# Kernel tuning notes

Measured on AMD Instinct MI355X. Metric: run time of the kernel, lower is better.

## Reference

```python
import jax, jax.numpy as jnp
import numpy as np

NUM_GRAPHS = 512
BN_EPS = 1e-5

def _lin(k, fin, fout):
    kw, kb = jax.random.split(k)
    s = 1.0 / np.sqrt(fin)
    return (jax.random.uniform(kw, (fin, fout), jnp.float32, -s, s),
            jax.random.uniform(kb, (fout,), jnp.float32, -s, s))

def setup_inputs() -> dict:
    key = jax.random.key(0)
    ks = jax.random.split(key, 16)
    N, E, F, C, H, O = 50000, 800000, 128, 256, 512, 768
    x = jax.random.normal(ks[0], (N, F), jnp.float32)
    edge_index = jax.random.randint(ks[1], (2, E), 0, N, jnp.int64)
    batch = jnp.sort(jax.random.randint(ks[2], (N,), 0, NUM_GRAPHS, jnp.int64))
    d = {"x": x, "edge_index": edge_index, "batch": batch}
    d["w1a"], d["b1a"] = _lin(ks[3], F, C)
    d["g1"], d["be1"] = jnp.ones((C,), jnp.float32), jnp.zeros((C,), jnp.float32)
    d["w1b"], d["b1b"] = _lin(ks[4], C, C)
    d["w2a"], d["b2a"] = _lin(ks[5], C, C)
    d["g2"], d["be2"] = jnp.ones((C,), jnp.float32), jnp.zeros((C,), jnp.float32)
    d["w2b"], d["b2b"] = _lin(ks[6], C, C)
    d["w3a"], d["b3a"] = _lin(ks[7], C, C)
    d["g3"], d["be3"] = jnp.ones((C,), jnp.float32), jnp.zeros((C,), jnp.float32)
    d["w3b"], d["b3b"] = _lin(ks[8], C, C)
    d["wh1"], d["bh1"] = _lin(ks[9], C, H)
    d["wh2"], d["bh2"] = _lin(ks[10], H, O)
    return d

def _bn(z, g, b):
    mu = jnp.mean(z, axis=0)
    var = jnp.mean((z - mu) ** 2, axis=0)  # biased var, torch BN training mode
    return (z - mu) * jax.lax.rsqrt(var + BN_EPS) * g + b

def _gin(x, edge_index, wa, ba, g, be, wb, bb, tanh_out):
    src, dst = edge_index[0], edge_index[1]
    agg = jax.ops.segment_sum(x[src], dst, num_segments=x.shape[0])
    h = x + agg  # eps = 0
    z = jax.nn.relu(_bn(h @ wa + ba, g, be))
    z = z @ wb + bb
    return jnp.tanh(z) if tanh_out else z

def reference(x, edge_index, batch,
              w1a, b1a, g1, be1, w1b, b1b,
              w2a, b2a, g2, be2, w2b, b2b,
              w3a, b3a, g3, be3, w3b, b3b,
              wh1, bh1, wh2, bh2):
    h = jax.nn.relu(_gin(x, edge_index, w1a, b1a, g1, be1, w1b, b1b, False))
    h = jax.nn.relu(_gin(h, edge_index, w2a, b2a, g2, be2, w2b, b2b, True))
    h = _gin(h, edge_index, w3a, b3a, g3, be3, w3b, b3b, True)
    # global mean pool over graphs
    sums = jax.ops.segment_sum(h, batch, num_segments=NUM_GRAPHS)
    cnt = jax.ops.segment_sum(jnp.ones((h.shape[0],), h.dtype), batch, num_segments=NUM_GRAPHS)
    pooled = sums / jnp.maximum(cnt, 1.0)[:, None]
    z = jax.nn.relu(pooled @ wh1 + bh1)
    return z @ wh2 + bh2
```

## Files before the change

kernel.cpp:

```cpp
#include <hip/hip_runtime.h>


typedef __attribute__((ext_vector_type(8))) short short8;
typedef __attribute__((ext_vector_type(4))) float f32x4;
typedef __attribute__((ext_vector_type(4))) unsigned short us4;
typedef __attribute__((ext_vector_type(8))) unsigned short us8;

__device__ __forceinline__ unsigned short f2bf(float f) {
  unsigned int b = __float_as_uint(f);
  unsigned int r = 0x7FFFu + ((b >> 16) & 1u);
  return (unsigned short)((b + r) >> 16);
}
__device__ __forceinline__ float bf2f(unsigned short u) {
  return __uint_as_float(((unsigned int)u) << 16);
}

__device__ __forceinline__ int sw8(int row) {
  return (row & 7) ^ ((row >> 3) & 7);
}

typedef const __attribute__((address_space(1))) unsigned int* gas1;
typedef __attribute__((address_space(3))) unsigned int* las3;
__device__ __forceinline__ void gload16(const void* g, void* l) {
  __builtin_amdgcn_global_load_lds((gas1)g, (las3)l, 16, 0, 0);
}

__device__ __forceinline__ size_t swz8_idx(int row, int k, int K) {
  int g = k >> 3;
  return (size_t)row * K + ((g >> 3) << 6) + ((((g & 7) ^ sw8(row)) << 3)) + (k & 7);
}

__global__ void k_histbounds(const int* __restrict__ ei, int* __restrict__ deg, int E,
                             int eb, const int* __restrict__ batch,
                             int* __restrict__ gs, int* __restrict__ ge, int N) {
  int b = blockIdx.x;
  if (b < eb) {
    int e = b * 256 + threadIdx.x;
    if (e < E) atomicAdd(&deg[ei[E + e]], 1);
  } else {
    int i = (b - eb) * 256 + threadIdx.x;
    if (i < N) {
      int bb = batch[i];
      if (i == 0 || batch[i - 1] != bb) gs[bb] = i;
      if (i == N - 1 || batch[i + 1] != bb) ge[bb] = i + 1;
    }
  }
}

__global__ __launch_bounds__(1024) void k_scan1(const int* __restrict__ deg,
                                                int* __restrict__ partial,
                                                int* __restrict__ bsum, int N) {
  __shared__ int sd[1024];
  int tid = threadIdx.x;
  int i = blockIdx.x * 1024 + tid;
  int v = (i < N) ? deg[i] : 0;
  sd[tid] = v;
  __syncthreads();
  for (int off = 1; off < 1024; off <<= 1) {
    int t = (tid >= off) ? sd[tid - off] : 0;
    __syncthreads();
    sd[tid] += t;
    __syncthreads();
  }
  if (i < N) partial[i] = sd[tid];
  if (tid == 1023) bsum[blockIdx.x] = sd[1023];
}

__global__ void k_scan2(int* __restrict__ bsum, int nb) {
  int l = threadIdx.x;
  int orig = (l < nb) ? bsum[l] : 0;
  int v = orig;
  for (int off = 1; off < 64; off <<= 1) {
    int t = __shfl_up(v, off);
    if (l >= off) v += t;
  }
  if (l < nb) bsum[l] = v - orig;
}

__global__ void k_scan3(const int* __restrict__ deg, const int* __restrict__ partial,
                        const int* __restrict__ bsum, int* __restrict__ rowptr,
                        int* __restrict__ cursor, int N) {
  int i = blockIdx.x * 256 + threadIdx.x;
  if (i >= N) return;
  int incl = partial[i] + bsum[i >> 10];
  rowptr[i + 1] = incl;
  cursor[i] = incl - deg[i];
  if (i == 0) rowptr[0] = 0;
}

__global__ void k_fill(const int* __restrict__ ei, int* __restrict__ cursor,
                       int* __restrict__ adj, int E) {
  int e = blockIdx.x * 256 + threadIdx.x;
  if (e >= E) return;
  int s = ei[e];
  int d = ei[E + e];
  int pos = atomicAdd(&cursor[d], 1);
  adj[pos] = s;
}

__global__ void k_xbf(const float* __restrict__ X, unsigned short* __restrict__ Xb,
                      int total) {
  int t = blockIdx.x * 256 + threadIdx.x;
  if (t * 8 >= total) return;
  const float4 v0 = *(const float4*)(X + t * 8);
  const float4 v1 = *(const float4*)(X + t * 8 + 4);
  us8 o;
  o[0] = f2bf(v0.x); o[1] = f2bf(v0.y); o[2] = f2bf(v0.z); o[3] = f2bf(v0.w);
  o[4] = f2bf(v1.x); o[5] = f2bf(v1.y); o[6] = f2bf(v1.z); o[7] = f2bf(v1.w);
  *(us8*)(Xb + t * 8) = o;
}

__global__ void k_prep_all(const float* __restrict__ w1a, const float* __restrict__ w1b,
                           const float* __restrict__ w2a, const float* __restrict__ w2b,
                           const float* __restrict__ w3a, const float* __restrict__ w3b,
                           const float* __restrict__ wh1, const float* __restrict__ wh2,
                           unsigned short* __restrict__ Hi, unsigned short* __restrict__ Lo) {
  int idx = blockIdx.x * 256 + threadIdx.x;
  const float* W; int K, Nout, lo_;
  if (idx < 32768)       { W = w1a; K = 128; Nout = 256; lo_ = 0; }
  else if (idx < 98304)  { W = w1b; K = 256; Nout = 256; lo_ = 32768; }
  else if (idx < 163840) { W = w2a; K = 256; Nout = 256; lo_ = 98304; }
  else if (idx < 229376) { W = w2b; K = 256; Nout = 256; lo_ = 163840; }
  else if (idx < 294912) { W = w3a; K = 256; Nout = 256; lo_ = 229376; }
  else if (idx < 360448) { W = w3b; K = 256; Nout = 256; lo_ = 294912; }
  else if (idx < 491520) { W = wh1; K = 256; Nout = 512; lo_ = 360448; }
  else                   { W = wh2; K = 512; Nout = 768; lo_ = 491520; }
  int li = idx - lo_;
  int n = li % Nout, k = li / Nout;
  float w = W[k * Nout + n];
  unsigned short h = f2bf(w);
  size_t oi = (size_t)lo_ + swz8_idx(n, k, K);
  Hi[oi] = h;
  Lo[oi] = f2bf(w - bf2f(h));
}

template <int C>
__global__ __launch_bounds__(256) void k_agg(const unsigned short* __restrict__ Xb,
                                             unsigned short* __restrict__ Hb,
                                             const int* __restrict__ rowptr,
                                             const int* __restrict__ adj, int N,
                                             float* __restrict__ statsZ) {
  if (blockIdx.x == 0) {
    statsZ[threadIdx.x] = 0.f;
    statsZ[256 + threadIdx.x] = 0.f;
  }
  int node = blockIdx.x * 4 + (threadIdx.x >> 6);
  if (node >= N) return;
  int lane = threadIdx.x & 63;
  int e0 = rowptr[node], e1 = rowptr[node + 1];
  if constexpr (C == 256) {
    us4 ov = *(const us4*)(Xb + (size_t)node * C + lane * 4);
    float a0 = bf2f(ov[0]), a1 = bf2f(ov[1]), a2 = bf2f(ov[2]), a3 = bf2f(ov[3]);
    int e = e0;
    for (; e + 4 <= e1; e += 4) {
      int s0 = adj[e], s1 = adj[e + 1], s2 = adj[e + 2], s3 = adj[e + 3];
      us4 v0 = *(const us4*)(Xb + (size_t)s0 * C + lane * 4);
      us4 v1 = *(const us4*)(Xb + (size_t)s1 * C + lane * 4);
      us4 v2 = *(const us4*)(Xb + (size_t)s2 * C + lane * 4);
      us4 v3 = *(const us4*)(Xb + (size_t)s3 * C + lane * 4);
      a0 += (bf2f(v0[0]) + bf2f(v1[0])) + (bf2f(v2[0]) + bf2f(v3[0]));
      a1 += (bf2f(v0[1]) + bf2f(v1[1])) + (bf2f(v2[1]) + bf2f(v3[1]));
      a2 += (bf2f(v0[2]) + bf2f(v1[2])) + (bf2f(v2[2]) + bf2f(v3[2]));
      a3 += (bf2f(v0[3]) + bf2f(v1[3])) + (bf2f(v2[3]) + bf2f(v3[3]));
    }
    for (; e < e1; ++e) {
      us4 v = *(const us4*)(Xb + (size_t)adj[e] * C + lane * 4);
      a0 += bf2f(v[0]); a1 += bf2f(v[1]); a2 += bf2f(v[2]); a3 += bf2f(v[3]);
    }
    us4 hv;
    hv[0] = f2bf(a0); hv[1] = f2bf(a1); hv[2] = f2bf(a2); hv[3] = f2bf(a3);
    size_t oi = (size_t)node * 256 + ((lane >> 4) << 6) +
                ((((lane >> 1) & 7) ^ sw8(node)) << 3) + ((lane & 1) << 2);
    *(us4*)(Hb + oi) = hv;
  } else {
    ushort2 ov = *(const ushort2*)(Xb + (size_t)node * C + lane * 2);
    float a0 = bf2f(ov.x), a1 = bf2f(ov.y);
    int e = e0;
    for (; e + 4 <= e1; e += 4) {
      int s0 = adj[e], s1 = adj[e + 1], s2 = adj[e + 2], s3 = adj[e + 3];
      ushort2 v0 = *(const ushort2*)(Xb + (size_t)s0 * C + lane * 2);
      ushort2 v1 = *(const ushort2*)(Xb + (size_t)s1 * C + lane * 2);
      ushort2 v2 = *(const ushort2*)(Xb + (size_t)s2 * C + lane * 2);
      ushort2 v3 = *(const ushort2*)(Xb + (size_t)s3 * C + lane * 2);
      a0 += (bf2f(v0.x) + bf2f(v1.x)) + (bf2f(v2.x) + bf2f(v3.x));
      a1 += (bf2f(v0.y) + bf2f(v1.y)) + (bf2f(v2.y) + bf2f(v3.y));
    }
    for (; e < e1; ++e) {
      ushort2 v = *(const ushort2*)(Xb + (size_t)adj[e] * C + lane * 2);
      a0 += bf2f(v.x); a1 += bf2f(v.y);
    }
    ushort2 hv = {f2bf(a0), f2bf(a1)};
    size_t oi = (size_t)node * 128 + ((lane >> 5) << 6) +
                ((((lane >> 2) & 7) ^ sw8(node)) << 3) + ((lane & 3) << 1);
    *(ushort2*)(Hb + oi) = hv;
  }
}

template <int EPI, bool STATS, bool OSPLIT, bool XSWZ, int ASRC, bool FULL, bool OBF16>
__global__ __launch_bounds__(256) void k_gemm(
    const unsigned short* __restrict__ AHb, const unsigned short* __restrict__ ALo,
    const unsigned short* __restrict__ Zb,
    int M, int K, int Nld, int mb, int per,
    const unsigned short* __restrict__ WHi, const unsigned short* __restrict__ WLo,
    const float* __restrict__ bias,
    const float* __restrict__ statsIn, const float* __restrict__ gvec,
    const float* __restrict__ bevec,
    float* __restrict__ Out, unsigned short* __restrict__ OutB,
    unsigned short* __restrict__ OHi, unsigned short* __restrict__ OLo,
    float* __restrict__ statsOut) {
  __shared__ unsigned short aHi[4096], bHi[8192];
  __shared__ unsigned short aLo[FULL ? 4096 : 64], bLo[FULL ? 8192 : 64];
  __shared__ float sBNsc[ASRC == 2 ? 256 : 1], sBNsh[ASRC == 2 ? 256 : 1];
  int bx, by;
  if constexpr (XSWZ) {
    int xcd = blockIdx.x & 7, slot = blockIdx.x >> 3;
    bx = xcd * per + (slot >> 1);
    by = slot & 1;
    if (bx >= mb) return;
  } else {
    bx = blockIdx.x;
    by = blockIdx.y;
  }
  const int tid = threadIdx.x;
  const int lane = tid & 63, w = tid >> 6;
  const int wm = w >> 1, wn = w & 1;
  const int m0 = bx * 64, n0 = by * 128;

  if constexpr (ASRC == 2) {
    float mu = statsIn[tid] / (float)M;
    float var = statsIn[256 + tid] / (float)M - mu * mu;
    float sc = gvec[tid] * rsqrtf(var + 1e-5f);
    sBNsc[tid] = sc;
    sBNsh[tid] = bevec[tid] - mu * sc;
  }

  f32x4 zero = {0.f, 0.f, 0.f, 0.f};
  f32x4 acc[2][4];
#pragma unroll
  for (int i = 0; i < 2; ++i)
#pragma unroll
    for (int j = 0; j < 4; ++j) acc[i][j] = zero;

  const int l8 = lane >> 3;
  const int s8 = lane & 7;

  us8 zr0, zr1;
  const unsigned short* zb0 = nullptr;
  const unsigned short* zb1 = nullptr;
  if constexpr (ASRC == 2) {
    int r0 = tid >> 3, r1 = 32 + (tid >> 3);
    int ra0 = m0 + r0; if (ra0 >= M) ra0 = M - 1;
    int ra1 = m0 + r1; if (ra1 >= M) ra1 = M - 1;
    zb0 = Zb + (size_t)ra0 * K + (tid & 7) * 8;
    zb1 = Zb + (size_t)ra1 * K + (tid & 7) * 8;
    zr0 = *(const us8*)(zb0);
    zr1 = *(const us8*)(zb1);
  }

  for (int kb = 0; kb < K; kb += 64) {
    __syncthreads();
    if constexpr (ASRC == 2) {
#pragma unroll
      for (int p = 0; p < 2; ++p) {
        int row = (p << 5) + (tid >> 3), gq = tid & 7;
        us8 zr = p ? zr1 : zr0;
        us8 hv;
#pragma unroll
        for (int jj = 0; jj < 8; ++jj) {
          int kc = kb + gq * 8 + jj;
          float o = fmaxf(bf2f(zr[jj]) * sBNsc[kc] + sBNsh[kc], 0.f);
          hv[jj] = f2bf(o);
        }
        int bo = row * 128 + ((gq ^ sw8(row)) << 4);
        *(us8*)((char*)aHi + bo) = hv;
      }
#pragma unroll
      for (int q = 0; q < 4; ++q) {
        int row = (w << 5) + (q << 3) + l8;
        size_t gb = (size_t)(n0 + row) * K + kb + s8 * 8;
        unsigned bo2 = (w << 12) + (q << 10);
        gload16(WHi + gb, (char*)bHi + bo2);
      }
    } else {
#pragma unroll
      for (int q = 0; q < 2; ++q) {
        int row = (w << 4) + (q << 3) + l8;
        int ra = m0 + row; if (ra >= M) ra = M - 1;
        size_t ga = (size_t)ra * K + kb + s8 * 8;
        unsigned boA = (w << 11) + (q << 10);
        gload16(AHb + ga, (char*)aHi + boA);
        if constexpr (FULL) gload16(ALo + ga, (char*)aLo + boA);
      }
#pragma unroll
      for (int q = 0; q < 4; ++q) {
        int row = (w << 5) + (q << 3) + l8;
        size_t gb = (size_t)(n0 + row) * K + kb + s8 * 8;
        unsigned bo2 = (w << 12) + (q << 10);
        gload16(WHi + gb, (char*)bHi + bo2);
        if constexpr (FULL) gload16(WLo + gb, (char*)bLo + bo2);
      }
    }
    __syncthreads();

    if constexpr (ASRC == 2) {
      if (kb + 64 < K) {
        zr0 = *(const us8*)(zb0 + kb + 64);
        zr1 = *(const us8*)(zb1 + kb + 64);
      }
    }

    const int j = lane >> 4;
#pragma unroll
    for (int kk = 0; kk < 2; ++kk) {
      int g = (kk << 2) + j;
      short8 bh[4], bl[4];
#pragma unroll
      for (int ni = 0; ni < 4; ++ni) {
        int r = wn * 64 + ni * 16 + (lane & 15);
        int bo = r * 128 + ((g ^ sw8(r)) << 4);
        bh[ni] = *(const short8*)((const char*)bHi + bo);
        if constexpr (FULL) bl[ni] = *(const short8*)((const char*)bLo + bo);
      }
#pragma unroll
      for (int mi = 0; mi < 2; ++mi) {
        int r = wm * 32 + mi * 16 + (lane & 15);
        int bo = r * 128 + ((g ^ sw8(r)) << 4);
        short8 ah = *(const short8*)((const char*)aHi + bo);
#pragma unroll
        for (int ni = 0; ni < 4; ++ni) {
          acc[mi][ni] = __builtin_amdgcn_mfma_f32_16x16x32_bf16(ah, bh[ni], acc[mi][ni], 0, 0, 0);
          if constexpr (FULL) {
            short8 al = *(const short8*)((const char*)aLo + bo);
            acc[mi][ni] = __builtin_amdgcn_mfma_f32_16x16x32_bf16(ah, bl[ni], acc[mi][ni], 0, 0, 0);
            acc[mi][ni] = __builtin_amdgcn_mfma_f32_16x16x32_bf16(al, bh[ni], acc[mi][ni], 0, 0, 0);
          }
        }
      }
    }
  }

#pragma unroll
  for (int ni = 0; ni < 4; ++ni) {
    int col = n0 + wn * 64 + ni * 16 + (lane & 15);
    float bc = bias[col];
    float s = 0.f, q = 0.f;
#pragma unroll
    for (int mi = 0; mi < 2; ++mi) {
      int rbase = m0 + wm * 32 + mi * 16 + (lane >> 4) * 4;
#pragma unroll
      for (int r = 0; r < 4; ++r) {
        int row = rbase + r;
        if (row < M) {
          float o = acc[mi][ni][r] + bc;
          if (STATS) { s += o; q += o * o; }
          if (OSPLIT) {
            o = fmaxf(o, 0.f);
            unsigned short h = f2bf(o);
            size_t oi = swz8_idx(row, col, Nld);
            OHi[oi] = h;
            OLo[oi] = f2bf(o - bf2f(h));
          } else {
            if (EPI == 1) o = fmaxf(o, 0.f);
            else if (EPI == 2) o = tanhf(o);
            else if (EPI == 3) o = fmaxf(tanhf(o), 0.f);
            if (OBF16) OutB[(size_t)row * Nld + col] = f2bf(o);
            else       Out[(size_t)row * Nld + col] = o;
          }
        }
      }
    }
    if (STATS) {
      s += __shfl_xor(s, 16); s += __shfl_xor(s, 32);
      q += __shfl_xor(q, 16); q += __shfl_xor(q, 32);
      if ((lane >> 4) == 0) {
        atomicAdd(&statsOut[col], s);
        atomicAdd(&statsOut[256 + col], q);
      }
    }
  }
}

__global__ __launch_bounds__(256) void k_pool(const unsigned short* __restrict__ Hb,
                                              const int* __restrict__ gs,
                                              const int* __restrict__ ge,
                                              unsigned short* __restrict__ PHi,
                                              unsigned short* __restrict__ PLo) {
  __shared__ float4 red[4][64];
  int gi = blockIdx.x;
  int s = gs[gi], e = ge[gi];
  int w = threadIdx.x >> 6, lane = threadIdx.x & 63;
  float4 acc = {0.f, 0.f, 0.f, 0.f};
  for (int r = s + w; r < e; r += 4) {
    us4 v = *(const us4*)(Hb + (size_t)r * 256 + lane * 4);
    acc.x += bf2f(v[0]); acc.y += bf2f(v[1]);
    acc.z += bf2f(v[2]); acc.w += bf2f(v[3]);
  }
  red[w][lane] = acc;
  __syncthreads();
  if (w == 0) {
    float4 a = red[0][lane], b = red[1][lane], c = red[2][lane], d = red[3][lane];
    float inv = 1.0f / fmaxf((float)(e - s), 1.0f);
    float vv[4] = {(a.x + b.x + c.x + d.x) * inv, (a.y + b.y + c.y + d.y) * inv,
                   (a.z + b.z + c.z + d.z) * inv, (a.w + b.w + c.w + d.w) * inv};
    us4 hv, lv;
#pragma unroll
    for (int j = 0; j < 4; ++j) {
      unsigned short h = f2bf(vv[j]);
      hv[j] = h;
      lv[j] = f2bf(vv[j] - bf2f(h));
    }
    size_t oi = (size_t)gi * 256 + ((lane >> 4) << 6) +
                ((((lane >> 1) & 7) ^ sw8(gi)) << 3) + ((lane & 1) << 2);
    *(us4*)(PHi + oi) = hv;
    *(us4*)(PLo + oi) = lv;
  }
}

extern "C" void kernel_launch(void* const* d_in, const int* in_sizes, int n_in,
                              void* d_out, int out_size, void* d_ws, size_t ws_size,
                              hipStream_t stream) {
  const float* x      = (const float*)d_in[0];
  const int* ei       = (const int*)d_in[1];
  const int* bat      = (const int*)d_in[2];
  const float* w1a = (const float*)d_in[3];  const float* b1a = (const float*)d_in[4];
  const float* g1  = (const float*)d_in[5];  const float* be1 = (const float*)d_in[6];
  const float* w1b = (const float*)d_in[7];  const float* b1b = (const float*)d_in[8];
  const float* w2a = (const float*)d_in[9];  const float* b2a = (const float*)d_in[10];
  const float* g2  = (const float*)d_in[11]; const float* be2 = (const float*)d_in[12];
  const float* w2b = (const float*)d_in[13]; const float* b2b = (const float*)d_in[14];
  const float* w3a = (const float*)d_in[15]; const float* b3a = (const float*)d_in[16];
  const float* g3  = (const float*)d_in[17]; const float* be3 = (const float*)d_in[18];
  const float* w3b = (const float*)d_in[19]; const float* b3b = (const float*)d_in[20];
  const float* wh1 = (const float*)d_in[21]; const float* bh1 = (const float*)d_in[22];
  const float* wh2 = (const float*)d_in[23]; const float* bh2 = (const float*)d_in[24];
  float* out = (float*)d_out;

  const int N = in_sizes[0] / 128;
  const int E = in_sizes[1] / 2;
  const int G = 512;

  char* ws = (char*)d_ws;
  size_t off = 0;
  auto alloc = [&](size_t bytes) {
    void* p = ws + off;
    off = (off + bytes + 255) & ~(size_t)255;
    return p;
  };
  unsigned short* hb = (unsigned short*)alloc((size_t)N * 256 * 2);
  unsigned short* zb = (unsigned short*)alloc((size_t)N * 256 * 2);
  unsigned short* ab = (unsigned short*)alloc((size_t)N * 256 * 2);
  unsigned short* xb = (unsigned short*)alloc((size_t)N * 128 * 2);
  int* adj     = (int*)alloc((size_t)E * 4);
  int* rowptr  = (int*)alloc((size_t)(N + 1) * 4);
  int* cursor  = (int*)alloc((size_t)N * 4);
  int* deg     = (int*)alloc((size_t)N * 4);
  int* partial = (int*)alloc((size_t)N * 4);
  int* bsum    = (int*)alloc(64 * 4);
  unsigned short* wHi = (unsigned short*)alloc(884736 * 2);
  unsigned short* wLo = (unsigned short*)alloc(884736 * 2);
  float* stats = (float*)alloc(512 * 4);
  int* gs      = (int*)alloc(G * 4);
  int* ge      = (int*)alloc(G * 4);
  unsigned short* poolHi = (unsigned short*)alloc((size_t)G * 256 * 2);
  unsigned short* poolLo = (unsigned short*)alloc((size_t)G * 256 * 2);
  unsigned short* thidHi = (unsigned short*)alloc((size_t)G * 512 * 2);
  unsigned short* thidLo = (unsigned short*)alloc((size_t)G * 512 * 2);

  const int o1a = 0, o1b = 32768, o2a = 98304, o2b = 163840, o3a = 229376, o3b = 294912;
  const int oh1 = 360448, oh2 = 491520;

  hipMemsetAsync(deg, 0, (size_t)N * 4, stream);
  hipMemsetAsync(gs, 0, (size_t)G * 4, stream);
  hipMemsetAsync(ge, 0, (size_t)G * 4, stream);

  int eb = (E + 255) / 256;
  int nbN = (N + 255) / 256;
  int nb1 = (N + 1023) >> 10;
  k_histbounds<<<eb + nbN, 256, 0, stream>>>(ei, deg, E, eb, bat, gs, ge, N);
  k_scan1<<<nb1, 1024, 0, stream>>>(deg, partial, bsum, N);
  k_scan2<<<1, 64, 0, stream>>>(bsum, nb1);
  k_scan3<<<nbN, 256, 0, stream>>>(deg, partial, bsum, rowptr, cursor, N);
  k_fill<<<eb, 256, 0, stream>>>(ei, cursor, adj, E);

  k_xbf<<<(N * 128 / 8 + 255) / 256, 256, 0, stream>>>(x, xb, N * 128);
  k_prep_all<<<3456, 256, 0, stream>>>(w1a, w1b, w2a, w2b, w3a, w3b, wh1, wh2, wHi, wLo);

  int nb4 = (N + 3) / 4;
  const int mb = (N + 63) / 64;
  const int per = (mb + 7) / 8;
  dim3 gg(per * 16);

  k_agg<128><<<nb4, 256, 0, stream>>>(xb, hb, rowptr, adj, N, stats);
  k_gemm<0, true, false, true, 0, false, true><<<gg, 256, 0, stream>>>(
      hb, nullptr, nullptr, N, 128, 256, mb, per, wHi + o1a, wLo + o1a, b1a,
      nullptr, nullptr, nullptr, nullptr, zb, nullptr, nullptr, stats);
  k_gemm<1, false, false, true, 2, false, true><<<gg, 256, 0, stream>>>(
      nullptr, nullptr, zb, N, 256, 256, mb, per, wHi + o1b, wLo + o1b, b1b,
      stats, g1, be1, nullptr, ab, nullptr, nullptr, nullptr);

  k_agg<256><<<nb4, 256, 0, stream>>>(ab, hb, rowptr, adj, N, stats);
  k_gemm<0, true, false, true, 0, false, true><<<gg, 256, 0, stream>>>(
      hb, nullptr, nullptr, N, 256, 256, mb, per, wHi + o2a, wLo + o2a, b2a,
      nullptr, nullptr, nullptr, nullptr, zb, nullptr, nullptr, stats);
  k_gemm<3, false, false, true, 2, false, true><<<gg, 256, 0, stream>>>(
      nullptr, nullptr, zb, N, 256, 256, mb, per, wHi + o2b, wLo + o2b, b2b,
      stats, g2, be2, nullptr, ab, nullptr, nullptr, nullptr);

  k_agg<256><<<nb4, 256, 0, stream>>>(ab, hb, rowptr, adj, N, stats);
  k_gemm<0, true, false, true, 0, false, true><<<gg, 256, 0, stream>>>(
      hb, nullptr, nullptr, N, 256, 256, mb, per, wHi + o3a, wLo + o3a, b3a,
      nullptr, nullptr, nullptr, nullptr, zb, nullptr, nullptr, stats);
  k_gemm<2, false, false, true, 2, false, true><<<gg, 256, 0, stream>>>(
      nullptr, nullptr, zb, N, 256, 256, mb, per, wHi + o3b, wLo + o3b, b3b,
      stats, g3, be3, nullptr, ab, nullptr, nullptr, nullptr);

  k_pool<<<G, 256, 0, stream>>>(ab, gs, ge, poolHi, poolLo);
  dim3 gh1(8, 4);
  k_gemm<1, false, true, false, 0, true, false><<<gh1, 256, 0, stream>>>(
      poolHi, poolLo, nullptr, G, 256, 512, 0, 0, wHi + oh1, wLo + oh1, bh1,
      nullptr, nullptr, nullptr, nullptr, nullptr, thidHi, thidLo, nullptr);
  dim3 gh2(8, 6);
  k_gemm<0, false, false, false, 0, true, false><<<gh2, 256, 0, stream>>>(
      thidHi, thidLo, nullptr, G, 512, 768, 0, 0, wHi + oh2, wLo + oh2, bh2,
      nullptr, nullptr, nullptr, out, nullptr, nullptr, nullptr, nullptr);
}
```

Measured before the change: 581.5 us.

## Prefetch next K-tile into registers for non-FULL GEMM path

For the non-FULL (single bf16) GEMM variants, A and B tiles are no longer fetched with direct global-to-LDS loads. Instead, the next K-tile is loaded into registers while the current tile is computed, then written to LDS at the top of the next iteration. This is meant to hide global load latency behind the MFMA work. In exchange it uses more registers, which can lower occupancy, and it adds an extra barrier per iteration. The FULL split-precision path keeps its previous direct-to-LDS loads.

```diff
diff --git a/kernel.cpp b/kernel.cpp
--- a/kernel.cpp
+++ b/kernel.cpp
@@ -232,6 +232,7 @@
     float sc = gvec[tid] * rsqrtf(var + 1e-5f);
     sBNsc[tid] = sc;
     sBNsh[tid] = bevec[tid] - mu * sc;
+    __syncthreads();
   }
 
   f32x4 zero = {0.f, 0.f, 0.f, 0.f};
@@ -244,44 +245,65 @@
   const int l8 = lane >> 3;
   const int s8 = lane & 7;
 
-  us8 zr0, zr1;
-  const unsigned short* zb0 = nullptr;
-  const unsigned short* zb1 = nullptr;
-  if constexpr (ASRC == 2) {
-    int r0 = tid >> 3, r1 = 32 + (tid >> 3);
-    int ra0 = m0 + r0; if (ra0 >= M) ra0 = M - 1;
-    int ra1 = m0 + r1; if (ra1 >= M) ra1 = M - 1;
-    zb0 = Zb + (size_t)ra0 * K + (tid & 7) * 8;
-    zb1 = Zb + (size_t)ra1 * K + (tid & 7) * 8;
-    zr0 = *(const us8*)(zb0);
-    zr1 = *(const us8*)(zb1);
+  us8 arg[2], brg[4];
+  const unsigned short* aptr[2];
+  const unsigned short* bptr[4];
+  if constexpr (!FULL) {
+    const unsigned short* asrc = (ASRC == 2) ? Zb : AHb;
+#pragma unroll
+    for (int p = 0; p < 2; ++p) {
+      int row = (p << 5) + (tid >> 3);
+      int ra = m0 + row; if (ra >= M) ra = M - 1;
+      aptr[p] = asrc + (size_t)ra * K + (tid & 7) * 8;
+      arg[p] = *(const us8*)(aptr[p]);
+    }
+#pragma unroll
+    for (int q = 0; q < 4; ++q) {
+      int row = (q << 5) + (tid >> 3);
+      bptr[q] = WHi + (size_t)(n0 + row) * K + (tid & 7) * 8;
+      brg[q] = *(const us8*)(bptr[q]);
+    }
   }
 
   for (int kb = 0; kb < K; kb += 64) {
-    __syncthreads();
-    if constexpr (ASRC == 2) {
-#pragma unroll
-      for (int p = 0; p < 2; ++p) {
-        int row = (p << 5) + (tid >> 3), gq = tid & 7;
-        us8 zr = p ? zr1 : zr0;
-        us8 hv;
-#pragma unroll
-        for (int jj = 0; jj < 8; ++jj) {
-          int kc = kb + gq * 8 + jj;
-          float o = fmaxf(bf2f(zr[jj]) * sBNsc[kc] + sBNsh[kc], 0.f);
-          hv[jj] = f2bf(o);
+    if constexpr (!FULL) {
+      if constexpr (ASRC == 2) {
+#pragma unroll
+        for (int p = 0; p < 2; ++p) {
+          int row = (p << 5) + (tid >> 3), gq = tid & 7;
+          us8 hv;
+#pragma unroll
+          for (int jj = 0; jj < 8; ++jj) {
+            int kc = kb + gq * 8 + jj;
+            float o = fmaxf(bf2f(arg[p][jj]) * sBNsc[kc] + sBNsh[kc], 0.f);
+            hv[jj] = f2bf(o);
+          }
+          int bo = row * 128 + ((gq ^ sw8(row)) << 4);
+          *(us8*)((char*)aHi + bo) = hv;
         }
-        int bo = row * 128 + ((gq ^ sw8(row)) << 4);
-        *(us8*)((char*)aHi + bo) = hv;
+      } else {
+#pragma unroll
+        for (int p = 0; p < 2; ++p) {
+          int row = (p << 5) + (tid >> 3);
+          int bo = row * 128 + ((tid & 7) << 4);
+          *(us8*)((char*)aHi + bo) = arg[p];
+        }
       }
 #pragma unroll
       for (int q = 0; q < 4; ++q) {
-        int row = (w << 5) + (q << 3) + l8;
-        size_t gb = (size_t)(n0 + row) * K + kb + s8 * 8;
-        unsigned bo2 = (w << 12) + (q << 10);
-        gload16(WHi + gb, (char*)bHi + bo2);
+        int row = (q << 5) + (tid >> 3);
+        int bo = row * 128 + ((tid & 7) << 4);
+        *(us8*)((char*)bHi + bo) = brg[q];
+      }
+      __syncthreads();
+      if (kb + 64 < K) {
+#pragma unroll
+        for (int p = 0; p < 2; ++p) arg[p] = *(const us8*)(aptr[p] + kb + 64);
+#pragma unroll
+        for (int q = 0; q < 4; ++q) brg[q] = *(const us8*)(bptr[q] + kb + 64);
       }
     } else {
+      __syncthreads();
 #pragma unroll
       for (int q = 0; q < 2; ++q) {
         int row = (w << 4) + (q << 3) + l8;
@@ -289,7 +311,7 @@
         size_t ga = (size_t)ra * K + kb + s8 * 8;
         unsigned boA = (w << 11) + (q << 10);
         gload16(AHb + ga, (char*)aHi + boA);
-        if constexpr (FULL) gload16(ALo + ga, (char*)aLo + boA);
+        gload16(ALo + ga, (char*)aLo + boA);
       }
 #pragma unroll
       for (int q = 0; q < 4; ++q) {
@@ -297,16 +319,9 @@
         size_t gb = (size_t)(n0 + row) * K + kb + s8 * 8;
         unsigned bo2 = (w << 12) + (q << 10);
         gload16(WHi + gb, (char*)bHi + bo2);
-        if constexpr (FULL) gload16(WLo + gb, (char*)bLo + bo2);
-      }
-    }
-    __syncthreads();
-
-    if constexpr (ASRC == 2) {
-      if (kb + 64 < K) {
-        zr0 = *(const us8*)(zb0 + kb + 64);
-        zr1 = *(const us8*)(zb1 + kb + 64);
-      }
+        gload16(WLo + gb, (char*)bLo + bo2);
+      }
+      __syncthreads();
     }
 
     const int j = lane >> 4;
@@ -337,6 +352,7 @@
         }
       }
     }
+    if constexpr (!FULL) __syncthreads();
   }
 
 #pragma unroll
```

New measurement: 577.3 us, median of 4. Within noise of the previous version (-0.7%).
